# Performance work log

Hardware: AMD Instinct MI355X
Metric: run time of the kernel (lower is better)

The kernel has to match this reference:

```python
import jax, jax.numpy as jnp
import numpy as np

HIDDEN = 2048
N_HEADS = 16
HEAD_DIM = HIDDEN // N_HEADS          # 128
KV_CHANNELS = 512
N_KV_HEADS = HIDDEN // KV_CHANNELS    # 4
ROTARY_BASE = 10000.0
ROTARY_DIM = HEAD_DIM                 # rotary_pct = 1.0
SCALE = HEAD_DIM ** -0.5
NEG = -1e9


def setup_inputs() -> dict:
    key = jax.random.key(0)
    k1, k2, k3 = jax.random.split(key, 3)
    B, S = 1, 2048
    hidden_states = jax.random.normal(k1, (B, S, HIDDEN), dtype=jnp.float32)
    # additive causal mask [B,1,S,S]
    causal = jnp.tril(jnp.ones((S, S), dtype=jnp.bool_))
    attention_mask = jnp.where(causal, 0.0, NEG).astype(jnp.float32)[None, None]
    position_ids = jnp.arange(S, dtype=jnp.int64 if jax.config.jax_enable_x64 else jnp.int32)[None].repeat(B, axis=0)
    # torch nn.Linear(in,out) stored as [in,out] so y = x @ W (no bias: no_bias=True)
    qkv_out = N_HEADS * HEAD_DIM + 2 * N_KV_HEADS * HEAD_DIM  # 3072
    W_attn = jax.random.normal(k2, (HIDDEN, qkv_out), dtype=jnp.float32) * (HIDDEN ** -0.5)
    W_proj = jax.random.normal(k3, (HIDDEN, HIDDEN), dtype=jnp.float32) * (HIDDEN ** -0.5)
    return {"hidden_states": hidden_states, "attention_mask": attention_mask,
            "position_ids": position_ids, "W_attn": W_attn, "W_proj": W_proj}


def _rotate_half(x):
    x1, x2 = jnp.split(x, 2, axis=-1)
    return jnp.concatenate([-x2, x1], axis=-1)


def _rope(q, k, position_ids):
    # Faithful to the source: emb = cat(sin(freqs), cos(freqs)); then use cos(emb), sin(emb)
    inv_freq = 1.0 / (ROTARY_BASE ** (jnp.arange(0, ROTARY_DIM, 2, dtype=jnp.float32) / ROTARY_DIM))
    t = position_ids.astype(jnp.float32)                      # [B,S]
    freqs = t[..., None] * inv_freq[None, None, :]            # [B,S,rd/2]
    emb = jnp.concatenate([jnp.sin(freqs), jnp.cos(freqs)], axis=-1)  # [B,S,rd]
    cos_e = jnp.cos(emb)[:, None, :, :]                       # [B,1,S,rd]
    sin_e = jnp.sin(emb)[:, None, :, :]
    q = q * cos_e + _rotate_half(q) * sin_e
    k = k * cos_e + _rotate_half(k) * sin_e
    return q, k


def reference(hidden_states, attention_mask, position_ids, W_attn, W_proj):
    B, S, _ = hidden_states.shape
    qkv = hidden_states @ W_attn                              # [B,S,3072]
    q_len = N_HEADS * HEAD_DIM
    kv_len = N_KV_HEADS * HEAD_DIM
    q, k, v = jnp.split(qkv, [q_len, q_len + kv_len], axis=-1)
    q = q.reshape(B, S, N_HEADS, HEAD_DIM).transpose(0, 2, 1, 3)      # [B,H,S,D]
    k = k.reshape(B, S, N_KV_HEADS, HEAD_DIM).transpose(0, 2, 1, 3)   # [B,Hkv,S,D]
    v = v.reshape(B, S, N_KV_HEADS, HEAD_DIM).transpose(0, 2, 1, 3)
    q, k = _rope(q, k, position_ids)
    # GQA: repeat_interleave over head dim
    rep = N_HEADS // N_KV_HEADS
    k = jnp.repeat(k, rep, axis=1)                            # [B,H,S,D]
    v = jnp.repeat(v, rep, axis=1)
    scores = jnp.einsum('bhqd,bhkd->bhqk', q, k) * SCALE + attention_mask
    probs = jax.nn.softmax(scores, axis=-1)
    attn = jnp.einsum('bhqk,bhkd->bhqd', probs, v)            # [B,H,S,D]
    attn = attn.transpose(0, 2, 1, 3).reshape(B, S, HIDDEN)
    return attn @ W_proj
```

## Files before the change

kernel.cpp:

```cpp
#include <hip/hip_runtime.h>


typedef short s16x8 __attribute__((ext_vector_type(8)));
typedef short s16x4 __attribute__((ext_vector_type(4)));
typedef float f32x4 __attribute__((ext_vector_type(4)));

#define MFMA16 __builtin_amdgcn_mfma_f32_16x16x32_bf16

static constexpr int S = 2048;
static constexpr int HID = 2048;
static constexpr int NH = 16;
static constexpr int HD = 128;
static constexpr int NKV = 4;
static constexpr int QKVN = 3072;
static constexpr float SCALE = 0.08838834764831845f;

__device__ __forceinline__ short f2bf(float f) {
  unsigned u = __float_as_uint(f);
  unsigned r = (u + 0x7FFFu + ((u >> 16) & 1u)) >> 16;
  return (short)r;
}
__device__ __forceinline__ float bf2f(short s) {
  return __uint_as_float(((unsigned)(unsigned short)s) << 16);
}
__device__ __forceinline__ void gload_lds16(const void* g, void* l) {
  __builtin_amdgcn_global_load_lds(
      (const __attribute__((address_space(1))) unsigned int*)g,
      (__attribute__((address_space(3))) unsigned int*)l, 16, 0, 0);
}

__global__ __launch_bounds__(256) void conv_bf16_kernel(
    const float* __restrict__ in, short* __restrict__ out) {
  int i = (blockIdx.x * 256 + threadIdx.x) * 4;
  float4 v = *(const float4*)(in + i);
  s16x4 o;
  o[0] = f2bf(v.x); o[1] = f2bf(v.y); o[2] = f2bf(v.z); o[3] = f2bf(v.w);
  *(s16x4*)(out + i) = o;
}

__global__ __launch_bounds__(256) void wtrans_kernel(
    const float* __restrict__ W, short* __restrict__ Wt, int R, int C) {
  __shared__ float tile[32][33];
  int c0 = blockIdx.x * 32, r0 = blockIdx.y * 32;
  int tx = threadIdx.x & 31, ty = threadIdx.x >> 5;
#pragma unroll
  for (int j = 0; j < 4; j++)
    tile[ty + j * 8][tx] = W[(size_t)(r0 + ty + j * 8) * C + c0 + tx];
  __syncthreads();
#pragma unroll
  for (int j = 0; j < 4; j++)
    Wt[(size_t)(c0 + ty + j * 8) * R + r0 + tx] = f2bf(tile[tx][ty + j * 8]);
}

__global__ __launch_bounds__(256) void vtrans_kernel(
    const short* __restrict__ qkv, short* __restrict__ Vt) {
  __shared__ short tile[32][34];
  int s0 = blockIdx.x * 32, d0 = blockIdx.y * 32, hk = blockIdx.z;
  int tx = threadIdx.x & 31, ty = threadIdx.x >> 5;
#pragma unroll
  for (int j = 0; j < 4; j++)
    tile[ty + j * 8][tx] =
        qkv[(size_t)(s0 + ty + j * 8) * QKVN + 2560 + hk * 128 + d0 + tx];
  __syncthreads();
#pragma unroll
  for (int j = 0; j < 4; j++)
    Vt[((size_t)hk * HD + d0 + ty + j * 8) * S + s0 + tx] = tile[tx][ty + j * 8];
}

__global__ __launch_bounds__(320) void rope_kernel(
    const short* __restrict__ qkv, short* __restrict__ Qb,
    short* __restrict__ Kb) {
  int s = blockIdx.x;
  int t = threadIdx.x;
  int hh = t >> 4;
  int li = t & 15;
  float p = (float)s;
  const short* row = qkv + (size_t)s * QKVN;
#pragma unroll
  for (int j = 0; j < 4; j++) {
    int i = li + 16 * j;
    float invf = __powf(10000.0f, -2.0f * (float)i / 128.0f);
    float fr = p * invf;
    float e1 = sinf(fr), e2 = cosf(fr);
    float c1 = cosf(e1), s1 = sinf(e1);
    float c2 = cosf(e2), s2 = sinf(e2);
    if (hh < NH) {
      const short* q = row + hh * HD;
      float a = bf2f(q[i]), b = bf2f(q[i + 64]);
      Qb[((size_t)hh * S + s) * HD + i] = f2bf(a * c1 - b * s1);
      Qb[((size_t)hh * S + s) * HD + i + 64] = f2bf(b * c2 + a * s2);
    } else {
      int hk = hh - NH;
      const short* k = row + HID + hk * HD;
      float a = bf2f(k[i]), b = bf2f(k[i + 64]);
      Kb[((size_t)hk * S + s) * HD + i] = f2bf(a * c1 - b * s1);
      Kb[((size_t)hk * S + s) * HD + i + 64] = f2bf(b * c2 + a * s2);
    }
  }
}

template <bool BF16OUT>
__global__ __launch_bounds__(256) void gemm_bt_kernel(
    const short* __restrict__ A, const short* __restrict__ Bt,
    void* __restrict__ Cout, int M, int N, int K) {
  __shared__ short As[128 * 32];
  __shared__ short Bs[128 * 32];
  int tid = threadIdx.x;
  int lane = tid & 63, wid = tid >> 6;
  int wr = wid >> 1, wc = wid & 1;
  int bm = blockIdx.y * 128, bn = blockIdx.x * 128;
  int srow = tid >> 2;
  int scol = (tid & 3) * 8;
  int rr = lane & 15;
  int kk = (lane >> 4) * 8;

  const short* Ag = A + (size_t)(bm + srow) * K + scol;
  const short* Bg = Bt + (size_t)(bn + srow) * K + scol;
  short* ldsA = As + wid * 512;
  short* ldsB = Bs + wid * 512;

  f32x4 acc[4][4] = {};

  for (int kb = 0; kb < K; kb += 32) {
    gload_lds16(Ag, ldsA);
    gload_lds16(Ag + (size_t)64 * K, ldsA + 2048);
    gload_lds16(Bg, ldsB);
    gload_lds16(Bg + (size_t)64 * K, ldsB + 2048);
    Ag += 32; Bg += 32;
    asm volatile("s_waitcnt vmcnt(0)" ::: "memory");
    __syncthreads();
    s16x8 af[4], bfr[4];
#pragma unroll
    for (int m = 0; m < 4; m++)
      af[m] = *(const s16x8*)&As[(wr * 64 + m * 16 + rr) * 32 + kk];
#pragma unroll
    for (int n = 0; n < 4; n++)
      bfr[n] = *(const s16x8*)&Bs[(wc * 64 + n * 16 + rr) * 32 + kk];
    __builtin_amdgcn_s_setprio(1);
#pragma unroll
    for (int m = 0; m < 4; m++)
#pragma unroll
      for (int n = 0; n < 4; n++)
        acc[m][n] = MFMA16(af[m], bfr[n], acc[m][n], 0, 0, 0);
    __builtin_amdgcn_s_setprio(0);
    __syncthreads();
  }

  int crow0 = bm + wr * 64 + (lane >> 4) * 4;
  int ccol0 = bn + wc * 64 + rr;
#pragma unroll
  for (int m = 0; m < 4; m++)
#pragma unroll
    for (int n = 0; n < 4; n++)
#pragma unroll
      for (int r = 0; r < 4; r++) {
        size_t idx = (size_t)(crow0 + m * 16 + r) * N + ccol0 + n * 16;
        if (BF16OUT) ((short*)Cout)[idx] = f2bf(acc[m][n][r]);
        else ((float*)Cout)[idx] = acc[m][n][r];
      }
}

__global__ __launch_bounds__(256) void attn_kernel(
    const short* __restrict__ Q, const short* __restrict__ K,
    const short* __restrict__ Vt, short* __restrict__ Ob) {
  __shared__ short Ks[2][8192];
  __shared__ short Vs[2][8192];
  __shared__ short Pl[4][16][72];
  int wid = threadIdx.x >> 6, lane = threadIdx.x & 63;
  int h = blockIdx.y;
  int qb = (int)gridDim.x - 1 - (int)blockIdx.x;
  int hk = h >> 2;
  int q0 = qb * 64 + wid * 16;
  int rr = lane & 15, rg = lane >> 4, r7 = rr & 7;

  const short* Qh = Q + ((size_t)h * S + q0) * HD;
  s16x8 qf[4];
#pragma unroll
  for (int kc = 0; kc < 4; kc++)
    qf[kc] = *(const s16x8*)(Qh + rr * HD + kc * 32 + rg * 8);

  const short* Kh = K + (size_t)hk * S * HD;
  const short* Vh = Vt + (size_t)hk * HD * S;

  size_t koff[4], voff[4];
  int kdst[4], vdst[4];
#pragma unroll
  for (int g = 0; g < 4; g++) {
    int kr = wid * 16 + g * 4 + (lane >> 4);
    koff[g] = (size_t)kr * 128 + 8 * ((lane & 15) ^ (kr & 7));
    kdst[g] = (wid * 16 + g * 4) * 128;
    int vr = wid * 32 + g * 8 + (lane >> 3);
    voff[g] = (size_t)vr * S + 8 * ((lane & 7) ^ (vr & 7));
    vdst[g] = (wid * 32 + g * 8) * 64;
  }

  f32x4 o[8] = {};
  float mrow[4], plr[4];
#pragma unroll
  for (int r = 0; r < 4; r++) { mrow[r] = -1e30f; plr[r] = 0.0f; }

#pragma unroll
  for (int g = 0; g < 4; g++) {
    gload_lds16(Kh + koff[g], &Ks[0][kdst[g]]);
    gload_lds16(Vh + voff[g], &Vs[0][vdst[g]]);
  }
  asm volatile("s_waitcnt vmcnt(0)" ::: "memory");
  __syncthreads();

  int nt = qb + 1;
  for (int t = 0; t < nt; ++t) {
    int buf = t & 1;
    if (t + 1 < nt) {
      size_t kvs = (size_t)(t + 1) * 64;
#pragma unroll
      for (int g = 0; g < 4; g++) {
        gload_lds16(Kh + kvs * 128 + koff[g], &Ks[buf ^ 1][kdst[g]]);
        gload_lds16(Vh + kvs + voff[g], &Vs[buf ^ 1][vdst[g]]);
      }
    }
    int kvb = t * 64;
    const short* Kb_ = Ks[buf];
    const short* Vb_ = Vs[buf];

    f32x4 sc4[4];
    __builtin_amdgcn_s_setprio(1);
#pragma unroll
    for (int c = 0; c < 4; c++) {
      f32x4 sacc = {};
#pragma unroll
      for (int kc = 0; kc < 4; kc++) {
        int chunk = (rg + kc * 4) ^ r7;
        s16x8 kf = *(const s16x8*)(Kb_ + (c * 16 + rr) * 128 + chunk * 8);
        sacc = MFMA16(qf[kc], kf, sacc, 0, 0, 0);
      }
      sc4[c] = sacc;
    }
    __builtin_amdgcn_s_setprio(0);

#pragma unroll
    for (int r = 0; r < 4; r++) {
      int qrow = q0 + rg * 4 + r;
      float v0 = sc4[0][r] * SCALE + ((kvb + rr) > qrow ? -1e9f : 0.0f);
      float v1 = sc4[1][r] * SCALE + ((kvb + 16 + rr) > qrow ? -1e9f : 0.0f);
      float v2 = sc4[2][r] * SCALE + ((kvb + 32 + rr) > qrow ? -1e9f : 0.0f);
      float v3 = sc4[3][r] * SCALE + ((kvb + 48 + rr) > qrow ? -1e9f : 0.0f);
      float pmax = fmaxf(fmaxf(v0, v1), fmaxf(v2, v3));
      unsigned long long bal = __ballot(pmax > mrow[r] + 8.0f);
      if ((bal >> (rg * 16)) & 0xFFFFull) {
        float mx = pmax;
#pragma unroll
        for (int d = 1; d < 16; d <<= 1) mx = fmaxf(mx, __shfl_xor(mx, d, 64));
        float mn = fmaxf(mrow[r], mx);
        float scl = __expf(mrow[r] - mn);
        mrow[r] = mn;
        plr[r] *= scl;
#pragma unroll
        for (int dc = 0; dc < 8; dc++) o[dc][r] *= scl;
      }
      float p0 = __expf(v0 - mrow[r]), p1 = __expf(v1 - mrow[r]);
      float p2 = __expf(v2 - mrow[r]), p3 = __expf(v3 - mrow[r]);
      plr[r] += (p0 + p1) + (p2 + p3);
      Pl[wid][rg * 4 + r][rr] = f2bf(p0);
      Pl[wid][rg * 4 + r][rr + 16] = f2bf(p1);
      Pl[wid][rg * 4 + r][rr + 32] = f2bf(p2);
      Pl[wid][rg * 4 + r][rr + 48] = f2bf(p3);
    }
    asm volatile("s_waitcnt lgkmcnt(0)" ::: "memory");
    __builtin_amdgcn_sched_barrier(0);
    s16x8 pf0 = *(const s16x8*)&Pl[wid][rr][rg * 8];
    s16x8 pf1 = *(const s16x8*)&Pl[wid][rr][32 + rg * 8];

    __builtin_amdgcn_s_setprio(1);
#pragma unroll
    for (int dc = 0; dc < 8; dc++) {
      int ch0 = rg ^ r7, ch1 = (rg + 4) ^ r7;
      s16x8 vf0 = *(const s16x8*)(Vb_ + (dc * 16 + rr) * 64 + ch0 * 8);
      s16x8 vf1 = *(const s16x8*)(Vb_ + (dc * 16 + rr) * 64 + ch1 * 8);
      o[dc] = MFMA16(pf0, vf0, o[dc], 0, 0, 0);
      o[dc] = MFMA16(pf1, vf1, o[dc], 0, 0, 0);
    }
    __builtin_amdgcn_s_setprio(0);

    asm volatile("s_waitcnt vmcnt(0)" ::: "memory");
    __syncthreads();
  }

#pragma unroll
  for (int r = 0; r < 4; r++) {
    float l = plr[r];
#pragma unroll
    for (int d = 1; d < 16; d <<= 1) l += __shfl_xor(l, d, 64);
    float inv = 1.0f / l;
    int srow = q0 + rg * 4 + r;
#pragma unroll
    for (int dc = 0; dc < 8; dc++)
      Ob[(size_t)srow * HID + h * HD + dc * 16 + rr] = f2bf(o[dc][r] * inv);
  }
}

extern "C" void kernel_launch(void* const* d_in, const int* in_sizes, int n_in,
                              void* d_out, int out_size, void* d_ws,
                              size_t ws_size, hipStream_t stream) {
  (void)in_sizes; (void)n_in; (void)out_size; (void)ws_size;
  const float* hidden = (const float*)d_in[0];
  const float* W_attn = (const float*)d_in[3];
  const float* W_proj = (const float*)d_in[4];
  float* out = (float*)d_out;

  char* ws = (char*)d_ws;
  short* hid_bf = (short*)(ws);
  short* wat    = (short*)(ws + 8388608);
  short* wpt    = (short*)(ws + 20971520);
  short* qkvb   = (short*)(ws + 29360128);
  short* Qb     = (short*)(ws + 41943040);
  short* Kb     = (short*)(ws + 50331648);
  short* Vt     = (short*)(ws + 52428800);
  short* Ab     = (short*)(ws + 54525952);

  hipLaunchKernelGGL(conv_bf16_kernel, dim3(4096), dim3(256), 0, stream,
                     hidden, hid_bf);
  hipLaunchKernelGGL(wtrans_kernel, dim3(96, 64), dim3(256), 0, stream,
                     W_attn, wat, HID, QKVN);
  hipLaunchKernelGGL(wtrans_kernel, dim3(64, 64), dim3(256), 0, stream,
                     W_proj, wpt, HID, HID);
  hipLaunchKernelGGL((gemm_bt_kernel<true>), dim3(QKVN / 128, S / 128),
                     dim3(256), 0, stream, hid_bf, wat, (void*)qkvb, S, QKVN,
                     HID);
  hipLaunchKernelGGL(rope_kernel, dim3(S), dim3(320), 0, stream, qkvb, Qb, Kb);
  hipLaunchKernelGGL(vtrans_kernel, dim3(S / 32, HD / 32, NKV), dim3(256), 0,
                     stream, qkvb, Vt);
  hipLaunchKernelGGL(attn_kernel, dim3(32, NH), dim3(256), 0, stream,
                     Qb, Kb, Vt, Ab);
  hipLaunchKernelGGL((gemm_bt_kernel<false>), dim3(HID / 128, S / 128),
                     dim3(256), 0, stream, Ab, wpt, (void*)out, S, HID, HID);
}
```

Before: 313.0 us.

## Fuse prep and rope kernels, double-buffer GEMM, fold scale into Q with exp2

Merges the bf16 conversion and the two weight transposes into one launch, and merges RoPE with the V transpose into another, to cut launch overhead. The GEMM gets double-buffered LDS so the next K-slice loads while the current one feeds MFMA. The attention kernel folds SCALE*log2(e) into Q so it can use exp2f, applies the causal mask only on the diagonal tile, and interleaves query blocks from both ends of the sequence to balance causal work across CUs. Pre-scaling Q before bf16 rounding slightly changes numerics, and the GEMM doubles its LDS use.

```diff
diff --git a/kernel.cpp b/kernel.cpp
--- a/kernel.cpp
+++ b/kernel.cpp
@@ -13,7 +13,7 @@
 static constexpr int HD = 128;
 static constexpr int NKV = 4;
 static constexpr int QKVN = 3072;
-static constexpr float SCALE = 0.08838834764831845f;
+static constexpr float QSCALE = 0.12751743f;
 
 __device__ __forceinline__ short f2bf(float f) {
   unsigned u = __float_as_uint(f);
@@ -29,19 +29,29 @@
       (__attribute__((address_space(3))) unsigned int*)l, 16, 0, 0);
 }
 
-__global__ __launch_bounds__(256) void conv_bf16_kernel(
-    const float* __restrict__ in, short* __restrict__ out) {
-  int i = (blockIdx.x * 256 + threadIdx.x) * 4;
-  float4 v = *(const float4*)(in + i);
-  s16x4 o;
-  o[0] = f2bf(v.x); o[1] = f2bf(v.y); o[2] = f2bf(v.z); o[3] = f2bf(v.w);
-  *(s16x4*)(out + i) = o;
-}
-
-__global__ __launch_bounds__(256) void wtrans_kernel(
-    const float* __restrict__ W, short* __restrict__ Wt, int R, int C) {
+__global__ __launch_bounds__(256) void prep_kernel(
+    const float* __restrict__ hidden, const float* __restrict__ Wa,
+    const float* __restrict__ Wp, short* __restrict__ hid_bf,
+    short* __restrict__ wat, short* __restrict__ wpt) {
+  int b = blockIdx.x;
+  if (b < 4096) {
+    int i = (b * 256 + threadIdx.x) * 4;
+    float4 v = *(const float4*)(hidden + i);
+    s16x4 o;
+    o[0] = f2bf(v.x); o[1] = f2bf(v.y); o[2] = f2bf(v.z); o[3] = f2bf(v.w);
+    *(s16x4*)(hid_bf + i) = o;
+    return;
+  }
   __shared__ float tile[32][33];
-  int c0 = blockIdx.x * 32, r0 = blockIdx.y * 32;
+  const float* W; short* Wt; int C, bx, by;
+  if (b < 10240) {
+    W = Wa; Wt = wat; C = QKVN;
+    int u = b - 4096; bx = u % 96; by = u / 96;
+  } else {
+    W = Wp; Wt = wpt; C = HID;
+    int u = b - 10240; bx = u & 63; by = u >> 6;
+  }
+  int c0 = bx * 32, r0 = by * 32;
   int tx = threadIdx.x & 31, ty = threadIdx.x >> 5;
 #pragma unroll
   for (int j = 0; j < 4; j++)
@@ -49,13 +59,44 @@
   __syncthreads();
 #pragma unroll
   for (int j = 0; j < 4; j++)
-    Wt[(size_t)(c0 + ty + j * 8) * R + r0 + tx] = f2bf(tile[tx][ty + j * 8]);
-}
-
-__global__ __launch_bounds__(256) void vtrans_kernel(
-    const short* __restrict__ qkv, short* __restrict__ Vt) {
+    Wt[(size_t)(c0 + ty + j * 8) * HID + r0 + tx] = f2bf(tile[tx][ty + j * 8]);
+}
+
+__global__ __launch_bounds__(256) void ropevt_kernel(
+    const short* __restrict__ qkv, short* __restrict__ Qb,
+    short* __restrict__ Kb, short* __restrict__ Vt) {
+  int b = blockIdx.x;
+  if (b < 2048) {
+    int s = b;
+    float p = (float)s;
+    const short* row = qkv + (size_t)s * QKVN;
+#pragma unroll
+    for (int j = 0; j < 5; j++) {
+      int w = j * 256 + threadIdx.x;
+      int hh = w >> 6, i = w & 63;
+      float fr = p * __powf(10000.0f, -(float)i / 64.0f);
+      float e1 = sinf(fr), e2 = cosf(fr);
+      float c1 = cosf(e1), s1 = sinf(e1);
+      float c2 = cosf(e2), s2 = sinf(e2);
+      if (hh < NH) {
+        const short* q = row + hh * HD;
+        float a = bf2f(q[i]), bb = bf2f(q[i + 64]);
+        Qb[((size_t)hh * S + s) * HD + i] = f2bf((a * c1 - bb * s1) * QSCALE);
+        Qb[((size_t)hh * S + s) * HD + i + 64] =
+            f2bf((bb * c2 + a * s2) * QSCALE);
+      } else {
+        int hk = hh - NH;
+        const short* k = row + HID + hk * HD;
+        float a = bf2f(k[i]), bb = bf2f(k[i + 64]);
+        Kb[((size_t)hk * S + s) * HD + i] = f2bf(a * c1 - bb * s1);
+        Kb[((size_t)hk * S + s) * HD + i + 64] = f2bf(bb * c2 + a * s2);
+      }
+    }
+    return;
+  }
   __shared__ short tile[32][34];
-  int s0 = blockIdx.x * 32, d0 = blockIdx.y * 32, hk = blockIdx.z;
+  int u = b - 2048;
+  int s0 = (u & 63) * 32, d0 = ((u >> 6) & 3) * 32, hk = u >> 8;
   int tx = threadIdx.x & 31, ty = threadIdx.x >> 5;
 #pragma unroll
   for (int j = 0; j < 4; j++)
@@ -67,44 +108,12 @@
     Vt[((size_t)hk * HD + d0 + ty + j * 8) * S + s0 + tx] = tile[tx][ty + j * 8];
 }
 
-__global__ __launch_bounds__(320) void rope_kernel(
-    const short* __restrict__ qkv, short* __restrict__ Qb,
-    short* __restrict__ Kb) {
-  int s = blockIdx.x;
-  int t = threadIdx.x;
-  int hh = t >> 4;
-  int li = t & 15;
-  float p = (float)s;
-  const short* row = qkv + (size_t)s * QKVN;
-#pragma unroll
-  for (int j = 0; j < 4; j++) {
-    int i = li + 16 * j;
-    float invf = __powf(10000.0f, -2.0f * (float)i / 128.0f);
-    float fr = p * invf;
-    float e1 = sinf(fr), e2 = cosf(fr);
-    float c1 = cosf(e1), s1 = sinf(e1);
-    float c2 = cosf(e2), s2 = sinf(e2);
-    if (hh < NH) {
-      const short* q = row + hh * HD;
-      float a = bf2f(q[i]), b = bf2f(q[i + 64]);
-      Qb[((size_t)hh * S + s) * HD + i] = f2bf(a * c1 - b * s1);
-      Qb[((size_t)hh * S + s) * HD + i + 64] = f2bf(b * c2 + a * s2);
-    } else {
-      int hk = hh - NH;
-      const short* k = row + HID + hk * HD;
-      float a = bf2f(k[i]), b = bf2f(k[i + 64]);
-      Kb[((size_t)hk * S + s) * HD + i] = f2bf(a * c1 - b * s1);
-      Kb[((size_t)hk * S + s) * HD + i + 64] = f2bf(b * c2 + a * s2);
-    }
-  }
-}
-
 template <bool BF16OUT>
 __global__ __launch_bounds__(256) void gemm_bt_kernel(
     const short* __restrict__ A, const short* __restrict__ Bt,
     void* __restrict__ Cout, int M, int N, int K) {
-  __shared__ short As[128 * 32];
-  __shared__ short Bs[128 * 32];
+  __shared__ short As[2][4096];
+  __shared__ short Bs[2][4096];
   int tid = threadIdx.x;
   int lane = tid & 63, wid = tid >> 6;
   int wr = wid >> 1, wc = wid & 1;
@@ -116,26 +125,35 @@
 
   const short* Ag = A + (size_t)(bm + srow) * K + scol;
   const short* Bg = Bt + (size_t)(bn + srow) * K + scol;
-  short* ldsA = As + wid * 512;
-  short* ldsB = Bs + wid * 512;
+  int ldst = wid * 512;
 
   f32x4 acc[4][4] = {};
 
-  for (int kb = 0; kb < K; kb += 32) {
-    gload_lds16(Ag, ldsA);
-    gload_lds16(Ag + (size_t)64 * K, ldsA + 2048);
-    gload_lds16(Bg, ldsB);
-    gload_lds16(Bg + (size_t)64 * K, ldsB + 2048);
-    Ag += 32; Bg += 32;
-    asm volatile("s_waitcnt vmcnt(0)" ::: "memory");
-    __syncthreads();
+  gload_lds16(Ag, &As[0][ldst]);
+  gload_lds16(Ag + (size_t)64 * K, &As[0][ldst + 2048]);
+  gload_lds16(Bg, &Bs[0][ldst]);
+  gload_lds16(Bg + (size_t)64 * K, &Bs[0][ldst + 2048]);
+  Ag += 32; Bg += 32;
+  asm volatile("s_waitcnt vmcnt(0)" ::: "memory");
+  __syncthreads();
+
+  int nk = K >> 5;
+  for (int i = 0; i < nk; ++i) {
+    int buf = i & 1;
+    if (i + 1 < nk) {
+      gload_lds16(Ag, &As[buf ^ 1][ldst]);
+      gload_lds16(Ag + (size_t)64 * K, &As[buf ^ 1][ldst + 2048]);
+      gload_lds16(Bg, &Bs[buf ^ 1][ldst]);
+      gload_lds16(Bg + (size_t)64 * K, &Bs[buf ^ 1][ldst + 2048]);
+      Ag += 32; Bg += 32;
+    }
     s16x8 af[4], bfr[4];
 #pragma unroll
     for (int m = 0; m < 4; m++)
-      af[m] = *(const s16x8*)&As[(wr * 64 + m * 16 + rr) * 32 + kk];
+      af[m] = *(const s16x8*)&As[buf][(wr * 64 + m * 16 + rr) * 32 + kk];
 #pragma unroll
     for (int n = 0; n < 4; n++)
-      bfr[n] = *(const s16x8*)&Bs[(wc * 64 + n * 16 + rr) * 32 + kk];
+      bfr[n] = *(const s16x8*)&Bs[buf][(wc * 64 + n * 16 + rr) * 32 + kk];
     __builtin_amdgcn_s_setprio(1);
 #pragma unroll
     for (int m = 0; m < 4; m++)
@@ -143,6 +161,7 @@
       for (int n = 0; n < 4; n++)
         acc[m][n] = MFMA16(af[m], bfr[n], acc[m][n], 0, 0, 0);
     __builtin_amdgcn_s_setprio(0);
+    asm volatile("s_waitcnt vmcnt(0)" ::: "memory");
     __syncthreads();
   }
 
@@ -167,8 +186,11 @@
   __shared__ short Vs[2][8192];
   __shared__ short Pl[4][16][72];
   int wid = threadIdx.x >> 6, lane = threadIdx.x & 63;
-  int h = blockIdx.y;
-  int qb = (int)gridDim.x - 1 - (int)blockIdx.x;
+  int gid = blockIdx.x;
+  int u = gid >> 1;
+  int h = u & 15;
+  int v = u >> 4;
+  int qb = (gid & 1) ? v : 31 - v;
   int hk = h >> 2;
   int q0 = qb * 64 + wid * 16;
   int rr = lane & 15, rg = lane >> 4, r7 = rr & 7;
@@ -207,10 +229,9 @@
   asm volatile("s_waitcnt vmcnt(0)" ::: "memory");
   __syncthreads();
 
-  int nt = qb + 1;
-  for (int t = 0; t < nt; ++t) {
+  for (int t = 0; t <= qb; ++t) {
     int buf = t & 1;
-    if (t + 1 < nt) {
+    if (t < qb) {
       size_t kvs = (size_t)(t + 1) * 64;
 #pragma unroll
       for (int g = 0; g < 4; g++) {
@@ -239,26 +260,30 @@
 
 #pragma unroll
     for (int r = 0; r < 4; r++) {
-      int qrow = q0 + rg * 4 + r;
-      float v0 = sc4[0][r] * SCALE + ((kvb + rr) > qrow ? -1e9f : 0.0f);
-      float v1 = sc4[1][r] * SCALE + ((kvb + 16 + rr) > qrow ? -1e9f : 0.0f);
-      float v2 = sc4[2][r] * SCALE + ((kvb + 32 + rr) > qrow ? -1e9f : 0.0f);
-      float v3 = sc4[3][r] * SCALE + ((kvb + 48 + rr) > qrow ? -1e9f : 0.0f);
+      float v0 = sc4[0][r], v1 = sc4[1][r];
+      float v2 = sc4[2][r], v3 = sc4[3][r];
+      if (t == qb) {
+        int qrow = q0 + rg * 4 + r;
+        v0 += (kvb + rr) > qrow ? -1e9f : 0.0f;
+        v1 += (kvb + 16 + rr) > qrow ? -1e9f : 0.0f;
+        v2 += (kvb + 32 + rr) > qrow ? -1e9f : 0.0f;
+        v3 += (kvb + 48 + rr) > qrow ? -1e9f : 0.0f;
+      }
       float pmax = fmaxf(fmaxf(v0, v1), fmaxf(v2, v3));
-      unsigned long long bal = __ballot(pmax > mrow[r] + 8.0f);
+      unsigned long long bal = __ballot(pmax > mrow[r] + 11.5f);
       if ((bal >> (rg * 16)) & 0xFFFFull) {
         float mx = pmax;
 #pragma unroll
         for (int d = 1; d < 16; d <<= 1) mx = fmaxf(mx, __shfl_xor(mx, d, 64));
         float mn = fmaxf(mrow[r], mx);
-        float scl = __expf(mrow[r] - mn);
+        float scl = exp2f(mrow[r] - mn);
         mrow[r] = mn;
         plr[r] *= scl;
 #pragma unroll
         for (int dc = 0; dc < 8; dc++) o[dc][r] *= scl;
       }
-      float p0 = __expf(v0 - mrow[r]), p1 = __expf(v1 - mrow[r]);
-      float p2 = __expf(v2 - mrow[r]), p3 = __expf(v3 - mrow[r]);
+      float p0 = exp2f(v0 - mrow[r]), p1 = exp2f(v1 - mrow[r]);
+      float p2 = exp2f(v2 - mrow[r]), p3 = exp2f(v3 - mrow[r]);
       plr[r] += (p0 + p1) + (p2 + p3);
       Pl[wid][rg * 4 + r][rr] = f2bf(p0);
       Pl[wid][rg * 4 + r][rr + 16] = f2bf(p1);
@@ -317,19 +342,14 @@
   short* Vt     = (short*)(ws + 52428800);
   short* Ab     = (short*)(ws + 54525952);
 
-  hipLaunchKernelGGL(conv_bf16_kernel, dim3(4096), dim3(256), 0, stream,
-                     hidden, hid_bf);
-  hipLaunchKernelGGL(wtrans_kernel, dim3(96, 64), dim3(256), 0, stream,
-                     W_attn, wat, HID, QKVN);
-  hipLaunchKernelGGL(wtrans_kernel, dim3(64, 64), dim3(256), 0, stream,
-                     W_proj, wpt, HID, HID);
+  hipLaunchKernelGGL(prep_kernel, dim3(14336), dim3(256), 0, stream,
+                     hidden, W_attn, W_proj, hid_bf, wat, wpt);
   hipLaunchKernelGGL((gemm_bt_kernel<true>), dim3(QKVN / 128, S / 128),
                      dim3(256), 0, stream, hid_bf, wat, (void*)qkvb, S, QKVN,
                      HID);
-  hipLaunchKernelGGL(rope_kernel, dim3(S), dim3(320), 0, stream, qkvb, Qb, Kb);
-  hipLaunchKernelGGL(vtrans_kernel, dim3(S / 32, HD / 32, NKV), dim3(256), 0,
-                     stream, qkvb, Vt);
-  hipLaunchKernelGGL(attn_kernel, dim3(32, NH), dim3(256), 0, stream,
+  hipLaunchKernelGGL(ropevt_kernel, dim3(3072), dim3(256), 0, stream,
+                     qkvb, Qb, Kb, Vt);
+  hipLaunchKernelGGL(attn_kernel, dim3(512), dim3(256), 0, stream,
                      Qb, Kb, Vt, Ab);
   hipLaunchKernelGGL((gemm_bt_kernel<false>), dim3(HID / 128, S / 128),
                      dim3(256), 0, stream, Ab, wpt, (void*)out, S, HID, HID);
```

Result: faster. 278.0 us (-11.2%).
